# Optimization experiments

Measured on AMD Instinct MI355X. Metric: run time of the kernel, lower is better.

## Reference

```python
import jax, jax.numpy as jnp
import numpy as np


def _bin_ids(start, length, S, P):
    # For adaptive max pool, output bin i over a region of length L covers
    # [floor(i*L/P), ceil((i+1)*L/P)). Adjacent bins overlap by at most one
    # element (when L >= P), so element h belongs to bins A(h)..B(h) with
    #   A(h) = floor(h*P/L),  B(h) = ceil((h+1)*P/L) - 1,  B - A <= 1.
    # Out-of-region positions are dumped into segment P.
    pos = jnp.arange(S, dtype=start.dtype)               # (S,)
    local = pos[None, :] - start[:, None]                # (N, S) local coord
    L = length[:, None]                                  # (N, 1)
    valid = (local >= 0) & (local < L)
    idA = jnp.where(valid, (local * P) // L, P)
    idB = jnp.where(valid, -((-((local + 1) * P)) // L) - 1, P)
    return idA, idB


def _roi_pool(feature_map, rois, PH, PW):
    C, H, W = feature_map.shape
    y, x, rH, rW = rois[:, 0], rois[:, 1], rois[:, 2], rois[:, 3]

    # ---- pool rows: (C,H,W) -> (N, PH, C, W) ----
    idA_h, idB_h = _bin_ids(y, rH, H, PH)                # (N, H) each
    fm_hcw = jnp.transpose(feature_map, (1, 0, 2))       # (H, C, W)
    seg_h = lambda ids: jax.ops.segment_max(fm_hcw, ids, num_segments=PH + 1)
    pooled_h = jnp.maximum(jax.vmap(seg_h)(idA_h), jax.vmap(seg_h)(idB_h))[:, :PH]

    # ---- pool cols: (N, PH, C, W) -> (N, PW, PH, C) ----
    idA_w, idB_w = _bin_ids(x, rW, W, PW)                # (N, W) each
    data_w = jnp.transpose(pooled_h, (0, 3, 1, 2))       # (N, W, PH, C)
    seg_w = lambda d, ids: jax.ops.segment_max(d, ids, num_segments=PW + 1)
    pooled = jnp.maximum(jax.vmap(seg_w)(data_w, idA_w),
                         jax.vmap(seg_w)(data_w, idB_w))[:, :PW]
    return jnp.transpose(pooled, (0, 3, 2, 1))           # (N, C, PH, PW)


def setup_inputs() -> dict:
    key = jax.random.key(0)
    k1, k2, k3, k4, k5 = jax.random.split(key, 5)
    C, H, W, N, PH, PW = 256, 128, 128, 256, 8, 8
    feature_map = jax.random.normal(k1, (C, H, W), dtype=jnp.float32)
    # valid ROIs: rH >= PH, rW >= PW, fully in-bounds
    rH = jax.random.randint(k2, (N,), PH, H + 1, dtype=jnp.int32)
    rW = jax.random.randint(k3, (N,), PW, W + 1, dtype=jnp.int32)
    y = (jax.random.uniform(k4, (N,)) * (H - rH + 1).astype(jnp.float32)).astype(jnp.int32)
    x = (jax.random.uniform(k5, (N,)) * (W - rW + 1).astype(jnp.float32)).astype(jnp.int32)
    rois = jnp.stack([y, x, rH, rW], axis=1)
    return {"feature_map": feature_map, "rois": rois, "PH": PH, "PW": PW}


def reference(feature_map, rois, PH, PW):
    return _roi_pool(feature_map, rois, PH, PW)
```

## Files before the change

kernel.cpp:

```cpp
#include <hip/hip_runtime.h>
#include <math.h>

#define C_ 256
#define H_ 128
#define W_ 128
#define PH_ 8
#define PW_ 8
#define HW_ (H_ * W_)
#define M3ROWS (H_ - 8 + 1)

typedef unsigned short u16;
typedef u16 u16x4 __attribute__((ext_vector_type(4)));
typedef u16 u16x8 __attribute__((ext_vector_type(8)));

__device__ __forceinline__ u16x8 kmax(u16x8 a, u16x8 b) {
    return __builtin_elementwise_max(a, b);
}

__device__ __forceinline__ u16 f32_to_key(float f) {
    unsigned u = __float_as_uint(f);
    unsigned r = (u + 0x7fffu + ((u >> 16) & 1u)) >> 16;
    u16 b = (u16)r;
    return (b & 0x8000u) ? (u16)~b : (u16)(b | 0x8000u);
}
__device__ __forceinline__ float key_to_f32(u16 k) {
    u16 b = (k & 0x8000u) ? (u16)(k & 0x7fffu) : (u16)~k;
    return __uint_as_float(((unsigned)b) << 16);
}

__global__ __launch_bounds__(256) void transpose_kernel(
    const float* __restrict__ fm, u16* __restrict__ fmt)
{
    __shared__ float tile[32 * 257];
    const int tid = threadIdx.x;
    const int g   = blockIdx.x & 7;
    const int hwb = blockIdx.x >> 3;
    const int c0  = g * 32;
    const int hw0 = hwb * 256;

    const int l    = tid & 63;
    const int crow = tid >> 6;
    const int sw   = (l >> 3) & 3;
    #pragma unroll
    for (int k = 0; k < 8; ++k) {
        const int c = crow + 4 * k;
        const float4 v = *(const float4*)(fm + (size_t)(c0 + c) * HW_ + hw0 + 4 * l);
        float* t = tile + c * 257 + 4 * l;
        t[(0 + sw) & 3] = v.x;
        t[(1 + sw) & 3] = v.y;
        t[(2 + sw) & 3] = v.z;
        t[(3 + sw) & 3] = v.w;
    }
    __syncthreads();

    u16* dst = fmt + (size_t)g * HW_ * 32;
    const int cq  = tid & 7;
    const int hwr = tid >> 3;
    #pragma unroll
    for (int m = 0; m < 8; ++m) {
        const int hw = hwr + 32 * m;
        const int o  = (hw & ~3) | (((hw & 3) + m) & 3);
        u16x4 w;
        w.x = f32_to_key(tile[(4 * cq + 0) * 257 + o]);
        w.y = f32_to_key(tile[(4 * cq + 1) * 257 + o]);
        w.z = f32_to_key(tile[(4 * cq + 2) * 257 + o]);
        w.w = f32_to_key(tile[(4 * cq + 3) * 257 + o]);
        *(u16x4*)(dst + (size_t)(hw0 + hw) * 32 + 4 * cq) = w;
    }
}

__global__ __launch_bounds__(256) void m3_kernel(
    const u16* __restrict__ fmt, u16* __restrict__ m3)
{
    const int bid  = blockIdx.x;
    const int g    = bid & 7;
    const int band = bid >> 3;
    const int i0   = band * 16;
    const int t    = threadIdx.x;
    const int co   = (t & 3) << 3;
    const int w0   = t >> 2;

    const u16* src = fmt + (size_t)g * HW_ * 32;
    u16*       dst = m3  + (size_t)g * M3ROWS * (W_ * 32);
    const size_t RS = (size_t)W_ * 32;

    #pragma unroll 1
    for (int seg = 0; seg < 2; ++seg) {
        const int w = w0 + 64 * seg;
        const size_t cofs = (size_t)w * 32 + co;
        u16x8 r[8];
        #pragma unroll
        for (int k = 0; k < 7; ++k)
            r[k] = *(const u16x8*)(src + (size_t)(i0 + k) * RS + cofs);
        #pragma unroll
        for (int j = 0; j < 16; ++j) {
            const int i = i0 + j;
            if (i < M3ROWS) {
                r[(j + 7) & 7] = *(const u16x8*)(src + (size_t)(i + 7) * RS + cofs);
                u16x8 m01 = kmax(r[0], r[1]);
                u16x8 m23 = kmax(r[2], r[3]);
                u16x8 m45 = kmax(r[4], r[5]);
                u16x8 m67 = kmax(r[6], r[7]);
                *(u16x8*)(dst + (size_t)i * RS + cofs) =
                    kmax(kmax(m01, m23), kmax(m45, m67));
            }
        }
    }
}

__global__ __launch_bounds__(256) void pool_kernel(
    const u16* __restrict__ fmt, const u16* __restrict__ m3,
    const int* __restrict__ rois, float* __restrict__ out, int N)
{
    const int bid  = blockIdx.x;
    const int cg   = bid & 7;
    const int phh  = (bid >> 3) & 1;
    const int half = (bid >> 4) & 1;
    const int n    = bid >> 5;

    const int wid  = threadIdx.x >> 6;
    const int lane = threadIdx.x & 63;
    const int pw   = half * 4 + wid;
    const int pg   = lane >> 2;
    const int co   = (lane & 3) << 3;

    const int4 roi = ((const int4*)rois)[n];
    const int y = roi.x, x = roi.y, rH = roi.z, rW = roi.w;

    const int ws = (pw * rW) >> 3;
    const int we = ((pw + 1) * rW + 7) >> 3;
    const int bw = we - ws;
    const int nsteps = (bw + 15) >> 4;

    const u16* plane   = fmt + (size_t)cg * HW_ * 32;
    const u16* m3plane = m3  + (size_t)cg * M3ROWS * (W_ * 32);
    const size_t RS = (size_t)W_ * 32;

    #pragma unroll
    for (int pj = 0; pj < 4; ++pj) {
        const int ph = phh * 4 + pj;
        const int hs = (ph * rH) >> 3;
        const int he = ((ph + 1) * rH + 7) >> 3;
        const int a  = y + hs;
        const int b  = y + he;
        const int L  = he - hs;

        u16x8 acc = {0, 0, 0, 0, 0, 0, 0, 0};

        for (int s = 0; s < nsteps; ++s) {
            const int col = ws + 16 * s + pg;
            if (col < we) {
                const size_t cofs = (size_t)(x + col) * 32 + co;
                if (L >= 8) {
                    u16x8 t0 = *(const u16x8*)(m3plane + (size_t)a * RS + cofs);
                    u16x8 t1 = *(const u16x8*)(m3plane + (size_t)(b - 8) * RS + cofs);
                    acc = kmax(acc, kmax(t0, t1));
                    if (L > 16)
                        acc = kmax(acc, *(const u16x8*)(plane + (size_t)(a + 8) * RS + cofs));
                } else if (L > 4) {
                    const u16* pp = plane + (size_t)a * RS + cofs;
                    const int last = L - 1;
                    u16x8 t0 = *(const u16x8*)(pp);
                    u16x8 t1 = *(const u16x8*)(pp + RS);
                    u16x8 t2 = *(const u16x8*)(pp + 2 * RS);
                    u16x8 t3 = *(const u16x8*)(pp + 3 * RS);
                    u16x8 t4 = *(const u16x8*)(pp + 4 * RS);
                    u16x8 t5 = *(const u16x8*)(pp + (size_t)min(5, last) * RS);
                    u16x8 t6 = *(const u16x8*)(pp + (size_t)min(6, last) * RS);
                    acc = kmax(acc, kmax(kmax(kmax(t0, t1), kmax(t2, t3)),
                                         kmax(kmax(t4, t5), t6)));
                } else {
                    const u16* pp = plane + (size_t)a * RS + cofs;
                    const int last = L - 1;
                    u16x8 t0 = *(const u16x8*)(pp);
                    u16x8 t1 = *(const u16x8*)(pp + (size_t)min(1, last) * RS);
                    u16x8 t2 = *(const u16x8*)(pp + (size_t)min(2, last) * RS);
                    u16x8 t3 = *(const u16x8*)(pp + (size_t)min(3, last) * RS);
                    acc = kmax(acc, kmax(kmax(t0, t1), kmax(t2, t3)));
                }
            }
        }

        union U { u16x8 v; unsigned u[4]; };
        U aa; aa.v = acc;
        #pragma unroll
        for (int mask = 4; mask <= 32; mask <<= 1) {
            U t;
            #pragma unroll
            for (int i = 0; i < 4; ++i) t.u[i] = __shfl_xor(aa.u[i], mask, 64);
            aa.v = __builtin_elementwise_max(aa.v, t.v);
        }

        if (pg == 0) {
            const int c = (cg << 5) + co;
            float* o = out + ((size_t)n * C_ + c) * (PH_ * PW_) + ph * PW_ + pw;
            #pragma unroll
            for (int i = 0; i < 8; ++i)
                o[(size_t)i * (PH_ * PW_)] = key_to_f32(aa.v[i]);
        }
    }
}

__global__ __launch_bounds__(256) void roi_pool_fallback(
    const float* __restrict__ fm, const int* __restrict__ rois,
    float* __restrict__ out, int N)
{
    const int wid  = threadIdx.x >> 6;
    const int lane = threadIdx.x & 63;
    const int bid  = blockIdx.x;
    const int xcd  = bid & 7;
    const int t    = bid >> 3;
    const int csub = t & 7;
    const int n    = t >> 3;
    if (n >= N) return;
    const int c = (xcd << 5) + (csub << 2) + wid;

    const int4 roi = ((const int4*)rois)[n];
    const int y = roi.x, x = roi.y, rH = roi.z, rW = roi.w;

    const float2* plane2 = (const float2*)(fm + (size_t)c * (H_ * W_));
    const int pw = lane & 7;
    const int j  = lane >> 3;
    const int ws = (pw * rW) >> 3;
    const int we = (((pw + 1) * rW) + 7) >> 3;

    #pragma unroll
    for (int ph = 0; ph < PH_; ++ph) {
        const int hs = (ph * rH) >> 3;
        const int he = ((ph + 1) * rH + 7) >> 3;
        const float2* p = plane2 + (size_t)(y + hs) * (W_ / 2) + lane;
        float m0 = -INFINITY, m1 = -INFINITY;
        int cnt = he - hs;
        while (cnt >= 2) {
            const float2 a = p[0];
            const float2 b = p[W_ / 2];
            p += W_; cnt -= 2;
            m0 = fmaxf(m0, fmaxf(a.x, b.x));
            m1 = fmaxf(m1, fmaxf(a.y, b.y));
        }
        if (cnt) { const float2 a = p[0]; m0 = fmaxf(m0, a.x); m1 = fmaxf(m1, a.y); }

        float rr = -INFINITY;
        #pragma unroll
        for (int k = 0; k < 3; ++k) {
            const int w  = ws + j + k * 8;
            const int wa = x + w;
            const float a = __shfl(m0, (wa >> 1) & 63, 64);
            const float b = __shfl(m1, (wa >> 1) & 63, 64);
            if (w < we) rr = fmaxf(rr, (wa & 1) ? b : a);
        }
        rr = fmaxf(rr, __shfl_xor(rr, 8, 64));
        rr = fmaxf(rr, __shfl_xor(rr, 16, 64));
        rr = fmaxf(rr, __shfl_xor(rr, 32, 64));
        if (lane < PW_) out[(((size_t)n * C_ + c) * PH_ + ph) * PW_ + lane] = rr;
    }
}

extern "C" void kernel_launch(void* const* d_in, const int* in_sizes, int n_in,
                              void* d_out, int out_size, void* d_ws, size_t ws_size,
                              hipStream_t stream) {
    const float* fm   = (const float*)d_in[0];
    const int*   rois = (const int*)d_in[1];
    float*       out  = (float*)d_out;
    const int N = in_sizes[1] / 4;

    const size_t fmt_bytes = (size_t)HW_ * C_ * sizeof(u16);
    const size_t m3_bytes  = (size_t)M3ROWS * W_ * C_ * sizeof(u16);
    if (ws_size >= fmt_bytes + m3_bytes) {
        u16* fmt = (u16*)d_ws;
        u16* m3  = (u16*)((char*)d_ws + fmt_bytes);
        transpose_kernel<<<dim3((HW_ / 256) * 8), 256, 0, stream>>>(fm, fmt);
        m3_kernel<<<dim3(64), 256, 0, stream>>>(fmt, m3);
        pool_kernel<<<dim3(N * 32), 256, 0, stream>>>(fmt, m3, rois, out, N);
    } else {
        roi_pool_fallback<<<dim3(64 * N), 256, 0, stream>>>(fm, rois, out, N);
    }
}
```

Measured before the change: 118.3 us.

## Precompute 2D sliding-window max tables and pool each bin with few lookups

Alongside the existing 8-row sliding max, the kernel now builds an 8-column sliding max and a combined 8x8 sliding max in extra workspace tables. The pool kernel is rewritten so each thread handles one (ph,pw) bin for 8 channels. It picks the matching table and covers the bin with at most 3x3 overlapping window lookups, replacing the per-column loops and cross-lane shuffle reductions. Output is staged through LDS so it can be written with contiguous float4 stores. The cost is an extra launch, double the workspace, and more table-building traffic, with scattered gathers in the pool kernel.

```diff
diff --git a/kernel.cpp b/kernel.cpp
--- a/kernel.cpp
+++ b/kernel.cpp
@@ -69,136 +69,143 @@
     }
 }
 
-__global__ __launch_bounds__(256) void m3_kernel(
-    const u16* __restrict__ fmt, u16* __restrict__ m3)
-{
-    const int bid  = blockIdx.x;
+__device__ __forceinline__ void vslide_body(
+    const u16* __restrict__ src, u16* __restrict__ dst, int bid)
+{
     const int g    = bid & 7;
-    const int band = bid >> 3;
+    const int band = (bid >> 3) & 7;
+    const int seg  = bid >> 6;
     const int i0   = band * 16;
     const int t    = threadIdx.x;
     const int co   = (t & 3) << 3;
-    const int w0   = t >> 2;
-
-    const u16* src = fmt + (size_t)g * HW_ * 32;
-    u16*       dst = m3  + (size_t)g * M3ROWS * (W_ * 32);
+    const int w    = (t >> 2) + 64 * seg;
+
+    const u16* s = src + (size_t)g * HW_ * 32;
+    u16*       d = dst + (size_t)g * HW_ * 32;
     const size_t RS = (size_t)W_ * 32;
-
-    #pragma unroll 1
-    for (int seg = 0; seg < 2; ++seg) {
-        const int w = w0 + 64 * seg;
-        const size_t cofs = (size_t)w * 32 + co;
-        u16x8 r[8];
-        #pragma unroll
-        for (int k = 0; k < 7; ++k)
-            r[k] = *(const u16x8*)(src + (size_t)(i0 + k) * RS + cofs);
-        #pragma unroll
-        for (int j = 0; j < 16; ++j) {
-            const int i = i0 + j;
-            if (i < M3ROWS) {
-                r[(j + 7) & 7] = *(const u16x8*)(src + (size_t)(i + 7) * RS + cofs);
-                u16x8 m01 = kmax(r[0], r[1]);
-                u16x8 m23 = kmax(r[2], r[3]);
-                u16x8 m45 = kmax(r[4], r[5]);
-                u16x8 m67 = kmax(r[6], r[7]);
-                *(u16x8*)(dst + (size_t)i * RS + cofs) =
-                    kmax(kmax(m01, m23), kmax(m45, m67));
-            }
-        }
-    }
-}
-
-__global__ __launch_bounds__(256) void pool_kernel(
-    const u16* __restrict__ fmt, const u16* __restrict__ m3,
-    const int* __restrict__ rois, float* __restrict__ out, int N)
+    const size_t cofs = (size_t)w * 32 + co;
+
+    u16x8 r[8];
+    #pragma unroll
+    for (int k = 0; k < 7; ++k)
+        r[k] = *(const u16x8*)(s + (size_t)(i0 + k) * RS + cofs);
+    #pragma unroll
+    for (int j = 0; j < 16; ++j) {
+        const int i = i0 + j;
+        if (i < M3ROWS) {
+            r[(j + 7) & 7] = *(const u16x8*)(s + (size_t)(i + 7) * RS + cofs);
+            u16x8 m01 = kmax(r[0], r[1]);
+            u16x8 m23 = kmax(r[2], r[3]);
+            u16x8 m45 = kmax(r[4], r[5]);
+            u16x8 m67 = kmax(r[6], r[7]);
+            *(u16x8*)(d + (size_t)i * RS + cofs) =
+                kmax(kmax(m01, m23), kmax(m45, m67));
+        }
+    }
+}
+
+__device__ __forceinline__ void mw_body(
+    const u16* __restrict__ src, u16* __restrict__ dst, int mbid)
+{
+    const int g     = mbid & 7;
+    const int hband = (mbid >> 3) & 1;
+    const int jseg  = mbid >> 4;
+    const int t     = threadIdx.x;
+    const int co    = (t & 3) << 3;
+    const int h     = hband * 64 + (t >> 2);
+
+    const int j0   = jseg * 31;
+    const int jcnt = min(31, M3ROWS - j0);
+
+    const size_t RS = (size_t)W_ * 32;
+    const u16* s = src + (size_t)g * HW_ * 32 + (size_t)h * RS + co;
+    u16*       d = dst + (size_t)g * HW_ * 32 + (size_t)h * RS + co;
+
+    u16x8 r[8];
+    #pragma unroll
+    for (int k = 0; k < 7; ++k)
+        r[k] = *(const u16x8*)(s + (size_t)(j0 + k) * 32);
+    #pragma unroll
+    for (int jj = 0; jj < 31; ++jj) {
+        if (jj < jcnt) {
+            r[(jj + 7) & 7] = *(const u16x8*)(s + (size_t)(j0 + jj + 7) * 32);
+            u16x8 m01 = kmax(r[0], r[1]);
+            u16x8 m23 = kmax(r[2], r[3]);
+            u16x8 m45 = kmax(r[4], r[5]);
+            u16x8 m67 = kmax(r[6], r[7]);
+            *(u16x8*)(d + (size_t)(j0 + jj) * 32) =
+                kmax(kmax(m01, m23), kmax(m45, m67));
+        }
+    }
+}
+
+__global__ __launch_bounds__(256) void k2_kernel(
+    const u16* __restrict__ fmt, u16* __restrict__ m3, u16* __restrict__ mw)
+{
+    const int bid = blockIdx.x;
+    if (bid < 128) vslide_body(fmt, m3, bid);
+    else           mw_body(fmt, mw, bid - 128);
+}
+
+__global__ __launch_bounds__(256) void k3_kernel(
+    const u16* __restrict__ mw, u16* __restrict__ m8)
+{
+    vslide_body(mw, m8, blockIdx.x);
+}
+
+__global__ __launch_bounds__(256) void pool2_kernel(
+    const u16* __restrict__ tabs, const int* __restrict__ rois,
+    float* __restrict__ out, int N)
 {
     const int bid  = blockIdx.x;
     const int cg   = bid & 7;
-    const int phh  = (bid >> 3) & 1;
-    const int half = (bid >> 4) & 1;
-    const int n    = bid >> 5;
-
-    const int wid  = threadIdx.x >> 6;
+    const int n    = bid >> 3;
+    const int w    = threadIdx.x >> 6;
     const int lane = threadIdx.x & 63;
-    const int pw   = half * 4 + wid;
-    const int pg   = lane >> 2;
-    const int co   = (lane & 3) << 3;
+    const int ph   = lane >> 3;
+    const int pw   = lane & 7;
+    const int co   = w << 3;
 
     const int4 roi = ((const int4*)rois)[n];
     const int y = roi.x, x = roi.y, rH = roi.z, rW = roi.w;
 
-    const int ws = (pw * rW) >> 3;
-    const int we = ((pw + 1) * rW + 7) >> 3;
-    const int bw = we - ws;
-    const int nsteps = (bw + 15) >> 4;
-
-    const u16* plane   = fmt + (size_t)cg * HW_ * 32;
-    const u16* m3plane = m3  + (size_t)cg * M3ROWS * (W_ * 32);
+    const int hs  = (ph * rH) >> 3;
+    const int he  = ((ph + 1) * rH + 7) >> 3;
+    const int ws_ = (pw * rW) >> 3;
+    const int we  = ((pw + 1) * rW + 7) >> 3;
+    const int a = y + hs, b = y + he, L = he - hs;
+    const int wa = x + ws_, wb = x + we, Wd = we - ws_;
+
+    const size_t T  = (size_t)HW_ * C_;
     const size_t RS = (size_t)W_ * 32;
-
-    #pragma unroll
-    for (int pj = 0; pj < 4; ++pj) {
-        const int ph = phh * 4 + pj;
-        const int hs = (ph * rH) >> 3;
-        const int he = ((ph + 1) * rH + 7) >> 3;
-        const int a  = y + hs;
-        const int b  = y + he;
-        const int L  = he - hs;
-
-        u16x8 acc = {0, 0, 0, 0, 0, 0, 0, 0};
-
-        for (int s = 0; s < nsteps; ++s) {
-            const int col = ws + 16 * s + pg;
-            if (col < we) {
-                const size_t cofs = (size_t)(x + col) * 32 + co;
-                if (L >= 8) {
-                    u16x8 t0 = *(const u16x8*)(m3plane + (size_t)a * RS + cofs);
-                    u16x8 t1 = *(const u16x8*)(m3plane + (size_t)(b - 8) * RS + cofs);
-                    acc = kmax(acc, kmax(t0, t1));
-                    if (L > 16)
-                        acc = kmax(acc, *(const u16x8*)(plane + (size_t)(a + 8) * RS + cofs));
-                } else if (L > 4) {
-                    const u16* pp = plane + (size_t)a * RS + cofs;
-                    const int last = L - 1;
-                    u16x8 t0 = *(const u16x8*)(pp);
-                    u16x8 t1 = *(const u16x8*)(pp + RS);
-                    u16x8 t2 = *(const u16x8*)(pp + 2 * RS);
-                    u16x8 t3 = *(const u16x8*)(pp + 3 * RS);
-                    u16x8 t4 = *(const u16x8*)(pp + 4 * RS);
-                    u16x8 t5 = *(const u16x8*)(pp + (size_t)min(5, last) * RS);
-                    u16x8 t6 = *(const u16x8*)(pp + (size_t)min(6, last) * RS);
-                    acc = kmax(acc, kmax(kmax(kmax(t0, t1), kmax(t2, t3)),
-                                         kmax(kmax(t4, t5), t6)));
-                } else {
-                    const u16* pp = plane + (size_t)a * RS + cofs;
-                    const int last = L - 1;
-                    u16x8 t0 = *(const u16x8*)(pp);
-                    u16x8 t1 = *(const u16x8*)(pp + (size_t)min(1, last) * RS);
-                    u16x8 t2 = *(const u16x8*)(pp + (size_t)min(2, last) * RS);
-                    u16x8 t3 = *(const u16x8*)(pp + (size_t)min(3, last) * RS);
-                    acc = kmax(acc, kmax(kmax(t0, t1), kmax(t2, t3)));
-                }
-            }
-        }
-
-        union U { u16x8 v; unsigned u[4]; };
-        U aa; aa.v = acc;
-        #pragma unroll
-        for (int mask = 4; mask <= 32; mask <<= 1) {
-            U t;
-            #pragma unroll
-            for (int i = 0; i < 4; ++i) t.u[i] = __shfl_xor(aa.u[i], mask, 64);
-            aa.v = __builtin_elementwise_max(aa.v, t.v);
-        }
-
-        if (pg == 0) {
-            const int c = (cg << 5) + co;
-            float* o = out + ((size_t)n * C_ + c) * (PH_ * PW_) + ph * PW_ + pw;
-            #pragma unroll
-            for (int i = 0; i < 8; ++i)
-                o[(size_t)i * (PH_ * PW_)] = key_to_f32(aa.v[i]);
-        }
-    }
+    const u16* pl = tabs + (size_t)cg * (HW_ * 32) + co;
+
+    const int rsp = (L >= 8), csp = (Wd >= 8);
+    const int rn = rsp ? ((L > 16) ? 3 : 2) : L;
+    const int cn = csp ? ((Wd > 16) ? 3 : 2) : Wd;
+    const u16* tab = pl + (size_t)rsp * T + (size_t)(csp * 2) * T;
+
+    u16x8 acc = {0, 0, 0, 0, 0, 0, 0, 0};
+    for (int r = 0; r < rn; ++r) {
+        const int row = rsp ? ((r == 0) ? a : (r == 1) ? (b - 8) : (a + 5))
+                            : (a + r);
+        const u16* rp = tab + (size_t)row * RS;
+        for (int c = 0; c < cn; ++c) {
+            const int col = csp ? ((c == 0) ? wa : (c == 1) ? (wb - 8) : (wa + 5))
+                                : (wa + c);
+            acc = kmax(acc, *(const u16x8*)(rp + (size_t)col * 32));
+        }
+    }
+
+    __shared__ float lds[2048];
+    float* lp = lds + (w << 9);
+    #pragma unroll
+    for (int i = 0; i < 8; ++i) lp[i * 64 + lane] = key_to_f32(acc[i]);
+    __syncthreads();
+    const float4* lp4 = (const float4*)lds + (w << 7);
+    float4* ob4 = (float4*)(out + ((size_t)n * C_ + (cg << 5) + co) * (PH_ * PW_));
+    ob4[lane]      = lp4[lane];
+    ob4[64 + lane] = lp4[64 + lane];
 }
 
 __global__ __launch_bounds__(256) void roi_pool_fallback(
@@ -264,14 +271,17 @@
     float*       out  = (float*)d_out;
     const int N = in_sizes[1] / 4;
 
-    const size_t fmt_bytes = (size_t)HW_ * C_ * sizeof(u16);
-    const size_t m3_bytes  = (size_t)M3ROWS * W_ * C_ * sizeof(u16);
-    if (ws_size >= fmt_bytes + m3_bytes) {
+    const size_t Tel  = (size_t)HW_ * C_;
+    const size_t need = 4 * Tel * sizeof(u16);
+    if (ws_size >= need) {
         u16* fmt = (u16*)d_ws;
-        u16* m3  = (u16*)((char*)d_ws + fmt_bytes);
+        u16* m3  = fmt + Tel;
+        u16* mw  = fmt + 2 * Tel;
+        u16* m8  = fmt + 3 * Tel;
         transpose_kernel<<<dim3((HW_ / 256) * 8), 256, 0, stream>>>(fm, fmt);
-        m3_kernel<<<dim3(64), 256, 0, stream>>>(fmt, m3);
-        pool_kernel<<<dim3(N * 32), 256, 0, stream>>>(fmt, m3, rois, out, N);
+        k2_kernel<<<dim3(192), 256, 0, stream>>>(fmt, m3, mw);
+        k3_kernel<<<dim3(128), 256, 0, stream>>>(mw, m8);
+        pool2_kernel<<<dim3(N * 8), 256, 0, stream>>>(fmt, rois, out, N);
     } else {
         roi_pool_fallback<<<dim3(64 * N), 256, 0, stream>>>(fm, rois, out, N);
     }
```

Measured after the change: 111.9 us. 5.4% less time.
